# Performance work log

Hardware: AMD Instinct MI355X
Metric: run time of the kernel (lower is better)

The kernel has to match this reference:

```python
import jax, jax.numpy as jnp
import numpy as np

B, N, D_IN, D_OUT = 4, 1024, 128, 64
SLOPE = 0.01  # LeakyReLU negative slope


def leaky_relu(x):
    return jnp.where(x >= 0, x, SLOPE * x)


def setup_inputs() -> dict:
    key = jax.random.key(0)
    k_x, k_m, k_w1, k_w2, k_a, k_l = jax.random.split(key, 6)
    x = jax.random.normal(k_x, (B, N, D_IN), dtype=jnp.float32)
    # binary adjacency mask; add self-loops so every row has >=1 neighbor
    mask = jax.random.bernoulli(k_m, 0.05, (B, N, N)).astype(jnp.float32)
    eye = jnp.eye(N, dtype=jnp.float32)[None]
    A_shape = jnp.maximum(mask, eye)
    w1 = jax.random.normal(k_w1, (D_IN, D_OUT), dtype=jnp.float32)
    w2 = jax.random.normal(k_w2, (D_IN, D_OUT), dtype=jnp.float32)
    a = jax.random.normal(k_a, (D_OUT,), dtype=jnp.float32)
    lin_w = jax.random.normal(k_l, (D_OUT, D_IN), dtype=jnp.float32) * (1.0 / np.sqrt(D_IN))
    return {"x": x, "A_shape": A_shape, "w1": w1, "w2": w2, "a": a, "lin_w": lin_w}


def reference(x, A_shape, w1, w2, a, lin_w):
    # x: [B,N,D_in], A_shape: [B,N,N] mask
    x1 = x @ w1            # [B,N,D_out]  (dst features)
    x2 = x @ w2            # [B,N,D_out]  (src features)
    # GATv2 additive score: leakyrelu(x1_i + x2_j) . a -> [B,N,N]
    S = leaky_relu(x1[:, :, None, :] + x2[:, None, :, :])
    S = jnp.einsum('bijd,d->bij', S, a)
    S = jnp.tanh(S / 8.0) * 8.0
    A = jnp.exp(S) * A_shape
    A = A / jnp.sum(A, axis=-1, keepdims=True)
    out = A @ x            # [B,N,D_in] weighted aggregate of raw features
    out = out @ lin_w.T    # [B,N,D_out]
    return leaky_relu(out)
```

## Files before the change

kernel.cpp:

```cpp
#include <hip/hip_runtime.h>
#include <math.h>

#define BB 4
#define NN 1024
#define DIN 128
#define DOUT 64
#define SLOPE 0.01f
#define RST 192
#define R1 16


__global__ __launch_bounds__(256, 2) void proj_kernel(
    const float* __restrict__ x, const float* __restrict__ w1,
    const float* __restrict__ w2, const float* __restrict__ lin_w,
    float* __restrict__ x12y) {
  int tid = threadIdx.x;
  int d = tid & 63;
  int g = tid >> 6;
  __shared__ __align__(16) float xl[R1][DIN];
  __shared__ float lwT[DIN][DOUT + 1];
  int row0 = blockIdx.x * R1;

  {
    const float4* xs = reinterpret_cast<const float4*>(x + (size_t)row0 * DIN);
    float4* xd = reinterpret_cast<float4*>(&xl[0][0]);
    xd[tid] = xs[tid];
    xd[tid + 256] = xs[tid + 256];
  }
#pragma unroll
  for (int i = 0; i < 32; ++i) {
    int idx = i * 256 + tid;
    lwT[idx & 127][idx >> 7] = lin_w[idx];
  }
  __syncthreads();

  float a1[4] = {0.f, 0.f, 0.f, 0.f};
  float a2[4] = {0.f, 0.f, 0.f, 0.f};
  float a3[4] = {0.f, 0.f, 0.f, 0.f};
  const float* w1c = w1 + d;
  const float* w2c = w2 + d;
#pragma unroll 4
  for (int k = 0; k < DIN; ++k) {
    float wv1 = w1c[k * DOUT];
    float wv2 = w2c[k * DOUT];
    float wv3 = lwT[k][d];
#pragma unroll
    for (int r = 0; r < 4; ++r) {
      float xv = xl[g * 4 + r][k];
      a1[r] = fmaf(xv, wv1, a1[r]);
      a2[r] = fmaf(xv, wv2, a2[r]);
      a3[r] = fmaf(xv, wv3, a3[r]);
    }
  }
#pragma unroll
  for (int r = 0; r < 4; ++r) {
    size_t o = (size_t)(row0 + g * 4 + r) * RST;
    x12y[o + d] = a1[r];
    x12y[o + DOUT + d] = a2[r];
    x12y[o + 2 * DOUT + d] = a3[r];
  }
}

__device__ __forceinline__ float fast_edge_exp(float sc) {
  float z = sc * 0.125f;
  z = fminf(10.f, fmaxf(-10.f, z));
  float u = __expf(2.f * z);
  float th = (u - 1.f) / (u + 1.f);
  return __expf(8.f * th);
}

__global__ __launch_bounds__(128, 8) void gat_row_kernel(
    const float* __restrict__ A_shape, const float* __restrict__ a_vec,
    const float* __restrict__ x12y, float* __restrict__ out) {
  int bi = blockIdx.x;
  int b = bi >> 10;
  int tid = threadIdx.x;
  int lane = tid & 63;
  int w = tid >> 6;

  __shared__ int eidx[1040];
  __shared__ float evals[1040];
  __shared__ __align__(16) float x1s[DOUT];
  __shared__ __align__(16) float avs[DOUT];
  __shared__ float aggh[2][DOUT];
  __shared__ float wsum[2];
  __shared__ int cnt[2];

  if (tid < DOUT) {
    x1s[tid] = x12y[(size_t)bi * RST + tid];
    avs[tid] = a_vec[tid];
  }

  const float* mask_row = A_shape + (size_t)bi * NN + w * 512;
  float mv[8];
#pragma unroll
  for (int c = 0; c < 8; ++c) mv[c] = mask_row[c * 64 + lane];
  int base = 0;
  int seg = w * 512;
#pragma unroll
  for (int c = 0; c < 8; ++c) {
    bool pred = (mv[c] != 0.f);
    unsigned long long m = __ballot(pred);
    int prefix = __popcll(m & ((1ull << lane) - 1ull));
    if (pred) eidx[seg + base + prefix] = w * 512 + c * 64 + lane;
    base += __popcll(m);
  }
  if (lane == 0) cnt[w] = base;
  __syncthreads();

  int nz0 = cnt[0], nz1 = cnt[1];
  int nzt = nz0 + nz1;
  int nzt16 = (nzt + 15) & ~15;
  if (tid < 16) {
    eidx[512 + nz1 + tid] = bi & (NN - 1);
    evals[512 + nz1 + tid] = 0.f;
  }
  __syncthreads();

  const float* x2b = x12y + (size_t)b * NN * RST + DOUT;
  int l16 = tid & 15;
  int grp = tid >> 4;
  float4 x1v = reinterpret_cast<const float4*>(x1s)[l16];
  float4 avv = reinterpret_cast<const float4*>(avs)[l16];
  float lsum = 0.f;
  for (int s = grp; s < nzt; s += 8) {
    int ps = (s < nz0) ? s : 512 + s - nz0;
    int j = eidx[ps];
    float4 x2v = *reinterpret_cast<const float4*>(
        x2b + (size_t)j * RST + l16 * 4);
    float z, sc = 0.f;
    z = x1v.x + x2v.x; sc = fmaf(z >= 0.f ? z : SLOPE * z, avv.x, sc);
    z = x1v.y + x2v.y; sc = fmaf(z >= 0.f ? z : SLOPE * z, avv.y, sc);
    z = x1v.z + x2v.z; sc = fmaf(z >= 0.f ? z : SLOPE * z, avv.z, sc);
    z = x1v.w + x2v.w; sc = fmaf(z >= 0.f ? z : SLOPE * z, avv.w, sc);
    sc += __shfl_xor(sc, 8, 16);
    sc += __shfl_xor(sc, 4, 16);
    sc += __shfl_xor(sc, 2, 16);
    sc += __shfl_xor(sc, 1, 16);
    if (l16 == 0) {
      float e = fast_edge_exp(sc);
      evals[ps] = e;
      lsum += e;
    }
  }

#pragma unroll
  for (int off = 32; off > 0; off >>= 1) lsum += __shfl_xor(lsum, off, 64);
  if (lane == 0) wsum[w] = lsum;
  __syncthreads();
  float inv = 1.f / (wsum[0] + wsum[1]);

  int d = tid & 63;
  int h = tid >> 6;
  const float* yb = x12y + (size_t)b * NN * RST + 2 * DOUT + d;
  float acc0 = 0.f, acc1 = 0.f;
  for (int s = 0; s < nzt16; s += 16) {
    int j[8];
    float wt[8];
#pragma unroll
    for (int r = 0; r < 8; ++r) {
      int ss = s + h + 2 * r;
      int ps = (ss < nz0) ? ss : 512 + ss - nz0;
      j[r] = eidx[ps];
      wt[r] = evals[ps];
    }
    float yv[8];
#pragma unroll
    for (int r = 0; r < 8; ++r) yv[r] = yb[(size_t)j[r] * RST];
#pragma unroll
    for (int r = 0; r < 8; r += 2) {
      acc0 = fmaf(wt[r], yv[r], acc0);
      acc1 = fmaf(wt[r + 1], yv[r + 1], acc1);
    }
  }
  aggh[h][d] = acc0 + acc1;
  __syncthreads();

  if (tid < DOUT) {
    float oo = (aggh[0][tid] + aggh[1][tid]) * inv;
    oo = oo >= 0.f ? oo : SLOPE * oo;
    out[(size_t)bi * DOUT + tid] = oo;
  }
}

extern "C" void kernel_launch(void* const* d_in, const int* in_sizes, int n_in,
                              void* d_out, int out_size, void* d_ws, size_t ws_size,
                              hipStream_t stream) {
  const float* x = (const float*)d_in[0];
  const float* A_shape = (const float*)d_in[1];
  const float* w1 = (const float*)d_in[2];
  const float* w2 = (const float*)d_in[3];
  const float* a = (const float*)d_in[4];
  const float* lin_w = (const float*)d_in[5];
  float* out = (float*)d_out;
  float* x12y = (float*)d_ws;

  proj_kernel<<<BB * NN / R1, 256, 0, stream>>>(x, w1, w2, lin_w, x12y);
  gat_row_kernel<<<BB * NN, 128, 0, stream>>>(A_shape, a, x12y, out);
}
```

Measured before the change: 99.84 us.

## Fuse edge score and aggregation into one pass; halve projection rows per block

The GAT row kernel now computes edge scores and accumulates the weighted aggregation in the same loop. Each wave handles 4 edges per step and broadcasts the exp weights by shuffle instead of writing them to shared memory and reading them back in a second loop. This removes the evals buffer, one barrier and a second pass over the neighbor indices, but every lane now computes exp redundantly and lsum is rescaled by 16. The projection kernel also drops from 16 rows per block to 8, doubling its block count to improve parallelism at the cost of reloading lin_w more often.

```diff
diff --git a/kernel.cpp b/kernel.cpp
--- a/kernel.cpp
+++ b/kernel.cpp
@@ -7,7 +7,7 @@
 #define DOUT 64
 #define SLOPE 0.01f
 #define RST 192
-#define R1 16
+#define R1 8
 
 
 __global__ __launch_bounds__(256, 2) void proj_kernel(
@@ -23,9 +23,7 @@
 
   {
     const float4* xs = reinterpret_cast<const float4*>(x + (size_t)row0 * DIN);
-    float4* xd = reinterpret_cast<float4*>(&xl[0][0]);
-    xd[tid] = xs[tid];
-    xd[tid + 256] = xs[tid + 256];
+    reinterpret_cast<float4*>(&xl[0][0])[tid] = xs[tid];
   }
 #pragma unroll
   for (int i = 0; i < 32; ++i) {
@@ -34,9 +32,9 @@
   }
   __syncthreads();
 
-  float a1[4] = {0.f, 0.f, 0.f, 0.f};
-  float a2[4] = {0.f, 0.f, 0.f, 0.f};
-  float a3[4] = {0.f, 0.f, 0.f, 0.f};
+  float a1[2] = {0.f, 0.f};
+  float a2[2] = {0.f, 0.f};
+  float a3[2] = {0.f, 0.f};
   const float* w1c = w1 + d;
   const float* w2c = w2 + d;
 #pragma unroll 4
@@ -45,16 +43,16 @@
     float wv2 = w2c[k * DOUT];
     float wv3 = lwT[k][d];
 #pragma unroll
-    for (int r = 0; r < 4; ++r) {
-      float xv = xl[g * 4 + r][k];
+    for (int r = 0; r < 2; ++r) {
+      float xv = xl[g * 2 + r][k];
       a1[r] = fmaf(xv, wv1, a1[r]);
       a2[r] = fmaf(xv, wv2, a2[r]);
       a3[r] = fmaf(xv, wv3, a3[r]);
     }
   }
 #pragma unroll
-  for (int r = 0; r < 4; ++r) {
-    size_t o = (size_t)(row0 + g * 4 + r) * RST;
+  for (int r = 0; r < 2; ++r) {
+    size_t o = (size_t)(row0 + g * 2 + r) * RST;
     x12y[o + d] = a1[r];
     x12y[o + DOUT + d] = a2[r];
     x12y[o + 2 * DOUT + d] = a3[r];
@@ -79,7 +77,6 @@
   int w = tid >> 6;
 
   __shared__ int eidx[1040];
-  __shared__ float evals[1040];
   __shared__ __align__(16) float x1s[DOUT];
   __shared__ __align__(16) float avs[DOUT];
   __shared__ float aggh[2][DOUT];
@@ -110,24 +107,33 @@
 
   int nz0 = cnt[0], nz1 = cnt[1];
   int nzt = nz0 + nz1;
-  int nzt16 = (nzt + 15) & ~15;
-  if (tid < 16) {
+  int nzt8 = (nzt + 7) & ~7;
+  if (tid < 8) {
     eidx[512 + nz1 + tid] = bi & (NN - 1);
-    evals[512 + nz1 + tid] = 0.f;
   }
   __syncthreads();
 
   const float* x2b = x12y + (size_t)b * NN * RST + DOUT;
+  const float* yb = x12y + (size_t)b * NN * RST + 2 * DOUT + lane;
   int l16 = tid & 15;
-  int grp = tid >> 4;
+  int g0 = lane >> 4;
   float4 x1v = reinterpret_cast<const float4*>(x1s)[l16];
   float4 avv = reinterpret_cast<const float4*>(avs)[l16];
   float lsum = 0.f;
-  for (int s = grp; s < nzt; s += 8) {
-    int ps = (s < nz0) ? s : 512 + s - nz0;
-    int j = eidx[ps];
+  float acc = 0.f;
+  for (int s0 = 0; s0 < nzt8; s0 += 8) {
+    int jj[4];
+#pragma unroll
+    for (int g2 = 0; g2 < 4; ++g2) {
+      int ss = s0 + 4 * w + g2;
+      int ps = (ss < nz0) ? ss : 512 + ss - nz0;
+      jj[g2] = eidx[ps];
+    }
+    float yv[4];
+#pragma unroll
+    for (int g2 = 0; g2 < 4; ++g2) yv[g2] = yb[(size_t)jj[g2] * RST];
     float4 x2v = *reinterpret_cast<const float4*>(
-        x2b + (size_t)j * RST + l16 * 4);
+        x2b + (size_t)jj[g0] * RST + l16 * 4);
     float z, sc = 0.f;
     z = x1v.x + x2v.x; sc = fmaf(z >= 0.f ? z : SLOPE * z, avv.x, sc);
     z = x1v.y + x2v.y; sc = fmaf(z >= 0.f ? z : SLOPE * z, avv.y, sc);
@@ -137,46 +143,24 @@
     sc += __shfl_xor(sc, 4, 16);
     sc += __shfl_xor(sc, 2, 16);
     sc += __shfl_xor(sc, 1, 16);
-    if (l16 == 0) {
-      float e = fast_edge_exp(sc);
-      evals[ps] = e;
-      lsum += e;
+    float e = fast_edge_exp(sc);
+    if (s0 + 4 * w + g0 >= nzt) e = 0.f;
+    lsum += e;
+#pragma unroll
+    for (int g2 = 0; g2 < 4; ++g2) {
+      float eg = __shfl(e, g2 * 16, 64);
+      acc = fmaf(eg, yv[g2], acc);
     }
   }
 
 #pragma unroll
   for (int off = 32; off > 0; off >>= 1) lsum += __shfl_xor(lsum, off, 64);
   if (lane == 0) wsum[w] = lsum;
-  __syncthreads();
-  float inv = 1.f / (wsum[0] + wsum[1]);
-
-  int d = tid & 63;
-  int h = tid >> 6;
-  const float* yb = x12y + (size_t)b * NN * RST + 2 * DOUT + d;
-  float acc0 = 0.f, acc1 = 0.f;
-  for (int s = 0; s < nzt16; s += 16) {
-    int j[8];
-    float wt[8];
-#pragma unroll
-    for (int r = 0; r < 8; ++r) {
-      int ss = s + h + 2 * r;
-      int ps = (ss < nz0) ? ss : 512 + ss - nz0;
-      j[r] = eidx[ps];
-      wt[r] = evals[ps];
-    }
-    float yv[8];
-#pragma unroll
-    for (int r = 0; r < 8; ++r) yv[r] = yb[(size_t)j[r] * RST];
-#pragma unroll
-    for (int r = 0; r < 8; r += 2) {
-      acc0 = fmaf(wt[r], yv[r], acc0);
-      acc1 = fmaf(wt[r + 1], yv[r + 1], acc1);
-    }
-  }
-  aggh[h][d] = acc0 + acc1;
+  aggh[w][lane] = acc;
   __syncthreads();
 
   if (tid < DOUT) {
+    float inv = 16.f / (wsum[0] + wsum[1]);
     float oo = (aggh[0][tid] + aggh[1][tid]) * inv;
     oo = oo >= 0.f ? oo : SLOPE * oo;
     out[(size_t)bi * DOUT + tid] = oo;
```

Measured after the change: 99.18 us. No clear change (-0.7%).
